# Performance work log

Measured on AMD Instinct MI355X. Metric: run time of the kernel, lower is better.

Reference implementation:

```python
import jax, jax.numpy as jnp
import numpy as np

N = 100000
E = 1600000
F_IN = 128
HID = 64


def setup_inputs() -> dict:
    key = jax.random.key(0)
    ks = jax.random.split(key, 8)
    x = jax.random.normal(ks[0], (N, F_IN), dtype=jnp.float32)
    edge_index = jax.random.randint(ks[1], (2, E), 0, N, dtype=jnp.int32)
    # GCNConv params: weight [in, out] (glorot-ish scale), bias [out]
    W1 = jax.random.normal(ks[2], (F_IN, HID), dtype=jnp.float32) / np.sqrt(F_IN)
    b1 = jnp.zeros((HID,), dtype=jnp.float32)
    W2 = jax.random.normal(ks[3], (HID, HID), dtype=jnp.float32) / np.sqrt(HID)
    b2 = jnp.zeros((HID,), dtype=jnp.float32)
    Wc = jax.random.normal(ks[4], (HID, 1), dtype=jnp.float32) / np.sqrt(HID)
    bc = jnp.zeros((1,), dtype=jnp.float32)
    return {"x": x, "edge_index": edge_index, "W1": W1, "b1": b1,
            "W2": W2, "b2": b2, "Wc": Wc, "bc": bc}


def _gcn_conv(x, src, dst, W, b):
    # PyG GCNConv: h = x @ W, then symmetric-normalized aggregation over
    # edges with self-loops: out[d] = sum_e deg^-1/2[s] deg^-1/2[d] h[s] + b
    n = x.shape[0]
    h = x @ W                                            # [N, out]
    deg = jax.ops.segment_sum(jnp.ones_like(dst, dtype=h.dtype), dst,
                              num_segments=n)            # in-degree incl. self-loops
    dinv = jnp.where(deg > 0, jax.lax.rsqrt(deg), 0.0)   # [N]
    norm = dinv[src] * dinv[dst]                         # [E+N]
    msg = h[src] * norm[:, None]                         # gather + scale
    out = jax.ops.segment_sum(msg, dst, num_segments=n)  # scatter-add
    return out + b


def reference(x, edge_index, W1, b1, W2, b2, Wc, bc):
    n = x.shape[0]
    loop = jnp.arange(n, dtype=edge_index.dtype)
    src = jnp.concatenate([edge_index[0], loop])  # add self-loops
    dst = jnp.concatenate([edge_index[1], loop])
    h = jax.nn.relu(_gcn_conv(x, src, dst, W1, b1))  # dropout in eval mode = identity
    h = jax.nn.relu(_gcn_conv(h, src, dst, W2, b2))
    return (h @ Wc + bc).squeeze(-1)  # [N]
```

## Files before the change

kernel.cpp:

```cpp
#include <hip/hip_runtime.h>


#define FIN 128
#define HIDDEN 64
#define NBUCK 196
#define CAP 9216
#define EPB 8192

typedef __attribute__((ext_vector_type(8))) short bf16x8;
typedef __attribute__((ext_vector_type(4))) float f32x4;

__device__ __forceinline__ unsigned f2bf_pair(float a, float b) {
    unsigned ua = __float_as_uint(a);
    unsigned ub = __float_as_uint(b);
    ua = (ua + 0x7FFFu + ((ua >> 16) & 1u)) >> 16;
    ub = (ub + 0x7FFFu + ((ub >> 16) & 1u)) & 0xFFFF0000u;
    return ua | ub;
}
__device__ __forceinline__ unsigned short f2bf1(float a) {
    unsigned u = __float_as_uint(a);
    return (unsigned short)((u + 0x7FFFu + ((u >> 16) & 1u)) >> 16);
}
#define BF_LO(u) __uint_as_float((u) << 16)
#define BF_HI(u) __uint_as_float((u) & 0xFFFF0000u)

__global__ __launch_bounds__(256) void k_scatter_direct(const int* __restrict__ src,
                                                        const int* __restrict__ dst,
                                                        int* __restrict__ bcursor,
                                                        int* __restrict__ pairs, int e) {
    __shared__ int h[NBUCK], base_s[NBUCK], cur[NBUCK];
    int tid = threadIdx.x;
    if (tid < NBUCK) { h[tid] = 0; cur[tid] = 0; }
    __syncthreads();
    int start = blockIdx.x * EPB;
#pragma unroll
    for (int i = 0; i < EPB / 256; i++) {
        int idx = start + tid + i * 256;
        if (idx < e) atomicAdd(&h[dst[idx] >> 9], 1);
    }
    __syncthreads();
    if (tid < NBUCK && h[tid] > 0) base_s[tid] = atomicAdd(&bcursor[tid], h[tid]);
    __syncthreads();
#pragma unroll
    for (int i = 0; i < EPB / 256; i++) {
        int idx = start + tid + i * 256;
        if (idx < e) {
            int d = dst[idx];
            int b = d >> 9;
            int pos = base_s[b] + atomicAdd(&cur[b], 1);
            if (pos < CAP) pairs[b * CAP + pos] = (src[idx] << 9) | (d & 511);
        }
    }
}

__global__ __launch_bounds__(256) void k_csr_bucket(const int* __restrict__ pairs,
                                                    const int* __restrict__ bcursor,
                                                    int2* __restrict__ rowinfo,
                                                    float* __restrict__ dinv,
                                                    int* __restrict__ csr_src, int n) {
    __shared__ int cnt[512];
    __shared__ int off[512];
    __shared__ int ws2[256];
    int tid = threadIdx.x;
    int b = blockIdx.x;
    int node0 = b << 9;
    cnt[tid] = 0; cnt[tid + 256] = 0;
    __syncthreads();
    int s0 = b * CAP;
    int s1 = s0 + min(bcursor[b], CAP);
    for (int i = s0 + tid; i < s1; i += 256) atomicAdd(&cnt[pairs[i] & 511], 1);
    __syncthreads();
    int c0 = cnt[2 * tid], c1 = cnt[2 * tid + 1];
    int tsum = c0 + c1;
    ws2[tid] = tsum;
    __syncthreads();
    for (int o = 1; o < 256; o <<= 1) {
        int x = 0;
        if (tid >= o) x = ws2[tid - o];
        __syncthreads();
        if (tid >= o) ws2[tid] += x;
        __syncthreads();
    }
    int excl = ws2[tid] - tsum;
    off[2 * tid] = excl;
    off[2 * tid + 1] = excl + c0;
    int n0 = node0 + 2 * tid, n1 = node0 + 2 * tid + 1;
    if (n0 < n) { rowinfo[n0] = make_int2(s0 + excl, c0);      dinv[n0] = rsqrtf((float)c0 + 1.0f); }
    if (n1 < n) { rowinfo[n1] = make_int2(s0 + excl + c0, c1); dinv[n1] = rsqrtf((float)c1 + 1.0f); }
    cnt[2 * tid] = 0; cnt[2 * tid + 1] = 0;
    __syncthreads();
    for (int i = s0 + tid; i < s1; i += 256) {
        int p = pairs[i];
        int l = p & 511;
        int pos = s0 + off[l] + atomicAdd(&cnt[l], 1);
        csr_src[pos] = p >> 9;
    }
}


__global__ __launch_bounds__(256) void k_mfma1(const float4* __restrict__ x4,
                                               const float* __restrict__ w1,
                                               const float* __restrict__ dinv,
                                               uint2* __restrict__ hsb, int n) {
    __shared__ unsigned short sW[64 * 136];
    int tid = threadIdx.x;
#pragma unroll
    for (int i = 0; i < 32; i++) {
        int idx = tid + i * 256;
        int k = idx >> 6, ch = idx & 63;
        sW[ch * 136 + k] = f2bf1(w1[idx]);
    }
    __syncthreads();
    int lane = tid & 63, wave = tid >> 6;
    int quad = lane >> 4, nl = lane & 15;
    int node = blockIdx.x * 64 + wave * 16 + nl;
    int ic = min(node, n - 1);
    const float4* px = x4 + (size_t)ic * 32 + quad * 2;
    bf16x8 bfr[4];
#pragma unroll
    for (int kc = 0; kc < 4; kc++) {
        float4 p = px[kc * 8];
        float4 q = px[kc * 8 + 1];
        union { unsigned u[4]; bf16x8 v; } t;
        t.u[0] = f2bf_pair(p.x, p.y); t.u[1] = f2bf_pair(p.z, p.w);
        t.u[2] = f2bf_pair(q.x, q.y); t.u[3] = f2bf_pair(q.z, q.w);
        bfr[kc] = t.v;
    }
    const bf16x8* sW8 = (const bf16x8*)sW;
    f32x4 a0 = {0.f, 0.f, 0.f, 0.f}, a1 = a0, a2 = a0, a3 = a0;
#pragma unroll
    for (int kc = 0; kc < 4; kc++) {
        int ko = kc * 4 + quad;
        bf16x8 w0 = sW8[(nl +  0) * 17 + ko];
        bf16x8 w1f = sW8[(nl + 16) * 17 + ko];
        bf16x8 w2f = sW8[(nl + 32) * 17 + ko];
        bf16x8 w3f = sW8[(nl + 48) * 17 + ko];
        a0 = __builtin_amdgcn_mfma_f32_16x16x32_bf16(w0,  bfr[kc], a0, 0, 0, 0);
        a1 = __builtin_amdgcn_mfma_f32_16x16x32_bf16(w1f, bfr[kc], a1, 0, 0, 0);
        a2 = __builtin_amdgcn_mfma_f32_16x16x32_bf16(w2f, bfr[kc], a2, 0, 0, 0);
        a3 = __builtin_amdgcn_mfma_f32_16x16x32_bf16(w3f, bfr[kc], a3, 0, 0, 0);
    }
    if (node < n) {
        float s = dinv[node];
        uint2* o = hsb + (size_t)node * 16 + quad;
        o[0]  = make_uint2(f2bf_pair(a0.x * s, a0.y * s), f2bf_pair(a0.z * s, a0.w * s));
        o[4]  = make_uint2(f2bf_pair(a1.x * s, a1.y * s), f2bf_pair(a1.z * s, a1.w * s));
        o[8]  = make_uint2(f2bf_pair(a2.x * s, a2.y * s), f2bf_pair(a2.z * s, a2.w * s));
        o[12] = make_uint2(f2bf_pair(a3.x * s, a3.y * s), f2bf_pair(a3.z * s, a3.w * s));
    }
}

__global__ __launch_bounds__(256) void k_mfma2(const float4* __restrict__ v4,
                                               const float* __restrict__ w2,
                                               const float* __restrict__ dinv,
                                               uint2* __restrict__ hsb, int n) {
    __shared__ unsigned short sW[64 * 72];
    int tid = threadIdx.x;
#pragma unroll
    for (int i = 0; i < 16; i++) {
        int idx = tid + i * 256;
        int k = idx >> 6, ch = idx & 63;
        sW[ch * 72 + k] = f2bf1(w2[idx]);
    }
    __syncthreads();
    int lane = tid & 63, wave = tid >> 6;
    int quad = lane >> 4, nl = lane & 15;
    int node = blockIdx.x * 64 + wave * 16 + nl;
    int ic = min(node, n - 1);
    const float4* px = v4 + (size_t)ic * 16 + quad * 2;
    bf16x8 bfr[2];
#pragma unroll
    for (int kc = 0; kc < 2; kc++) {
        float4 p = px[kc * 8];
        float4 q = px[kc * 8 + 1];
        union { unsigned u[4]; bf16x8 v; } t;
        t.u[0] = f2bf_pair(p.x, p.y); t.u[1] = f2bf_pair(p.z, p.w);
        t.u[2] = f2bf_pair(q.x, q.y); t.u[3] = f2bf_pair(q.z, q.w);
        bfr[kc] = t.v;
    }
    const bf16x8* sW8 = (const bf16x8*)sW;
    f32x4 a0 = {0.f, 0.f, 0.f, 0.f}, a1 = a0, a2 = a0, a3 = a0;
#pragma unroll
    for (int kc = 0; kc < 2; kc++) {
        int ko = kc * 4 + quad;
        bf16x8 w0 = sW8[(nl +  0) * 9 + ko];
        bf16x8 w1f = sW8[(nl + 16) * 9 + ko];
        bf16x8 w2f = sW8[(nl + 32) * 9 + ko];
        bf16x8 w3f = sW8[(nl + 48) * 9 + ko];
        a0 = __builtin_amdgcn_mfma_f32_16x16x32_bf16(w0,  bfr[kc], a0, 0, 0, 0);
        a1 = __builtin_amdgcn_mfma_f32_16x16x32_bf16(w1f, bfr[kc], a1, 0, 0, 0);
        a2 = __builtin_amdgcn_mfma_f32_16x16x32_bf16(w2f, bfr[kc], a2, 0, 0, 0);
        a3 = __builtin_amdgcn_mfma_f32_16x16x32_bf16(w3f, bfr[kc], a3, 0, 0, 0);
    }
    if (node < n) {
        float s = dinv[node];
        uint2* o = hsb + (size_t)node * 16 + quad;
        o[0]  = make_uint2(f2bf_pair(a0.x * s, a0.y * s), f2bf_pair(a0.z * s, a0.w * s));
        o[4]  = make_uint2(f2bf_pair(a1.x * s, a1.y * s), f2bf_pair(a1.z * s, a1.w * s));
        o[8]  = make_uint2(f2bf_pair(a2.x * s, a2.y * s), f2bf_pair(a2.z * s, a2.w * s));
        o[12] = make_uint2(f2bf_pair(a3.x * s, a3.y * s), f2bf_pair(a3.z * s, a3.w * s));
    }
}

__global__ __launch_bounds__(256) void k_agg1_fin(const int2* __restrict__ rowinfo,
                                                  const int* __restrict__ csr_src,
                                                  const uint4* __restrict__ hsb4,
                                                  const float* __restrict__ dinv,
                                                  const float4* __restrict__ b1_4,
                                                  float4* __restrict__ v4out, int n) {
    int lane = threadIdx.x & 63;
    int node = (blockIdx.x * 256 + threadIdx.x) >> 4;
    if (node >= n) return;
    int el = (lane >> 3) & 1, cq = lane & 7;
    int2 rpd = rowinfo[node];
    int start = rpd.x, deg = rpd.y;
    int end = start + deg;
    float4 accA = make_float4(0.f, 0.f, 0.f, 0.f), accB = accA;
    int nr = (deg + 3) >> 2;
    for (int r = 0; r < nr; r++) {
        int base = start + (r << 2);
        int e0 = base + el;
        int e1 = base + 2 + el;
        int s0 = csr_src[min(e0, end - 1)];
        int s1 = csr_src[min(e1, end - 1)];
        float m0 = (e0 < end) ? 1.f : 0.f;
        float m1 = (e1 < end) ? 1.f : 0.f;
        uint4 g0 = hsb4[(size_t)s0 * 8 + cq];
        uint4 g1 = hsb4[(size_t)s1 * 8 + cq];
        accA.x += m0 * BF_LO(g0.x) + m1 * BF_LO(g1.x);
        accA.y += m0 * BF_HI(g0.x) + m1 * BF_HI(g1.x);
        accA.z += m0 * BF_LO(g0.y) + m1 * BF_LO(g1.y);
        accA.w += m0 * BF_HI(g0.y) + m1 * BF_HI(g1.y);
        accB.x += m0 * BF_LO(g0.z) + m1 * BF_LO(g1.z);
        accB.y += m0 * BF_HI(g0.z) + m1 * BF_HI(g1.z);
        accB.z += m0 * BF_LO(g0.w) + m1 * BF_LO(g1.w);
        accB.w += m0 * BF_HI(g0.w) + m1 * BF_HI(g1.w);
    }
    accA.x += __shfl_xor(accA.x, 8); accA.y += __shfl_xor(accA.y, 8);
    accA.z += __shfl_xor(accA.z, 8); accA.w += __shfl_xor(accA.w, 8);
    accB.x += __shfl_xor(accB.x, 8); accB.y += __shfl_xor(accB.y, 8);
    accB.z += __shfl_xor(accB.z, 8); accB.w += __shfl_xor(accB.w, 8);
    if (el == 0) {
        uint4 g = hsb4[(size_t)node * 8 + cq];
        float s = dinv[node];
        float4 bA = b1_4[cq * 2], bB = b1_4[cq * 2 + 1];
        float4 vA, vB;
        vA.x = fmaxf(s * (accA.x + BF_LO(g.x)) + bA.x, 0.f);
        vA.y = fmaxf(s * (accA.y + BF_HI(g.x)) + bA.y, 0.f);
        vA.z = fmaxf(s * (accA.z + BF_LO(g.y)) + bA.z, 0.f);
        vA.w = fmaxf(s * (accA.w + BF_HI(g.y)) + bA.w, 0.f);
        vB.x = fmaxf(s * (accB.x + BF_LO(g.z)) + bB.x, 0.f);
        vB.y = fmaxf(s * (accB.y + BF_HI(g.z)) + bB.y, 0.f);
        vB.z = fmaxf(s * (accB.z + BF_LO(g.w)) + bB.z, 0.f);
        vB.w = fmaxf(s * (accB.w + BF_HI(g.w)) + bB.w, 0.f);
        v4out[(size_t)node * 16 + cq * 2] = vA;
        v4out[(size_t)node * 16 + cq * 2 + 1] = vB;
    }
}

__global__ __launch_bounds__(256) void k_agg2_head(const int2* __restrict__ rowinfo,
                                                   const int* __restrict__ csr_src,
                                                   const uint4* __restrict__ hsb4,
                                                   const float* __restrict__ dinv,
                                                   const float4* __restrict__ b2_4,
                                                   const float4* __restrict__ wc_4,
                                                   const float* __restrict__ bc,
                                                   float* __restrict__ out, int n) {
    int lane = threadIdx.x & 63;
    int node = (blockIdx.x * 256 + threadIdx.x) >> 4;
    if (node >= n) return;
    int el = (lane >> 3) & 1, cq = lane & 7;
    int2 rpd = rowinfo[node];
    int start = rpd.x, deg = rpd.y;
    int end = start + deg;
    float4 accA = make_float4(0.f, 0.f, 0.f, 0.f), accB = accA;
    int nr = (deg + 3) >> 2;
    for (int r = 0; r < nr; r++) {
        int base = start + (r << 2);
        int e0 = base + el;
        int e1 = base + 2 + el;
        int s0 = csr_src[min(e0, end - 1)];
        int s1 = csr_src[min(e1, end - 1)];
        float m0 = (e0 < end) ? 1.f : 0.f;
        float m1 = (e1 < end) ? 1.f : 0.f;
        uint4 g0 = hsb4[(size_t)s0 * 8 + cq];
        uint4 g1 = hsb4[(size_t)s1 * 8 + cq];
        accA.x += m0 * BF_LO(g0.x) + m1 * BF_LO(g1.x);
        accA.y += m0 * BF_HI(g0.x) + m1 * BF_HI(g1.x);
        accA.z += m0 * BF_LO(g0.y) + m1 * BF_LO(g1.y);
        accA.w += m0 * BF_HI(g0.y) + m1 * BF_HI(g1.y);
        accB.x += m0 * BF_LO(g0.z) + m1 * BF_LO(g1.z);
        accB.y += m0 * BF_HI(g0.z) + m1 * BF_HI(g1.z);
        accB.z += m0 * BF_LO(g0.w) + m1 * BF_LO(g1.w);
        accB.w += m0 * BF_HI(g0.w) + m1 * BF_HI(g1.w);
    }
    accA.x += __shfl_xor(accA.x, 8); accA.y += __shfl_xor(accA.y, 8);
    accA.z += __shfl_xor(accA.z, 8); accA.w += __shfl_xor(accA.w, 8);
    accB.x += __shfl_xor(accB.x, 8); accB.y += __shfl_xor(accB.y, 8);
    accB.z += __shfl_xor(accB.z, 8); accB.w += __shfl_xor(accB.w, 8);
    uint4 g = hsb4[(size_t)node * 8 + cq];
    float s = dinv[node];
    float4 bA = b2_4[cq * 2], bB = b2_4[cq * 2 + 1];
    float4 wA = wc_4[cq * 2], wB = wc_4[cq * 2 + 1];
    float t = fmaxf(s * (accA.x + BF_LO(g.x)) + bA.x, 0.f) * wA.x
            + fmaxf(s * (accA.y + BF_HI(g.x)) + bA.y, 0.f) * wA.y
            + fmaxf(s * (accA.z + BF_LO(g.y)) + bA.z, 0.f) * wA.z
            + fmaxf(s * (accA.w + BF_HI(g.y)) + bA.w, 0.f) * wA.w
            + fmaxf(s * (accB.x + BF_LO(g.z)) + bB.x, 0.f) * wB.x
            + fmaxf(s * (accB.y + BF_HI(g.z)) + bB.y, 0.f) * wB.y
            + fmaxf(s * (accB.z + BF_LO(g.w)) + bB.z, 0.f) * wB.z
            + fmaxf(s * (accB.w + BF_HI(g.w)) + bB.w, 0.f) * wB.w;
    t += __shfl_xor(t, 1);
    t += __shfl_xor(t, 2);
    t += __shfl_xor(t, 4);
    if ((lane & 15) == 0) out[node] = t + bc[0];
}

extern "C" void kernel_launch(void* const* d_in, const int* in_sizes, int n_in,
                              void* d_out, int out_size, void* d_ws, size_t ws_size,
                              hipStream_t stream) {
    const float* x  = (const float*)d_in[0];
    const int*   ei = (const int*)d_in[1];
    const float* W1 = (const float*)d_in[2];
    const float* b1 = (const float*)d_in[3];
    const float* W2 = (const float*)d_in[4];
    const float* b2 = (const float*)d_in[5];
    const float* Wc = (const float*)d_in[6];
    const float* bc = (const float*)d_in[7];
    int n = in_sizes[0] / FIN;
    int e = in_sizes[1] / 2;
    const int* srcv = ei;
    const int* dstv = ei + e;

    char* ws = (char*)d_ws;
    float* dinv    = (float*)(ws + 0);
    int2*  rowinfo = (int2*)(ws + (512u << 10));
    int*   csr_src = (int*)(ws + 1536u * 1024);
    int*   bcursor = (int*)(ws + 8800u * 1024);
    uint2* hsb     = (uint2*)(ws + (9u << 20));
    float* v       = (float*)(ws + (22u << 20));
    int*   pairs   = (int*)v;

    int nb_sc   = (e + EPB - 1) / EPB;
    int nb_rows = (n + 63) / 64;
    int nb_agg  = (n + 15) / 16;

    hipMemsetAsync(bcursor, 0, NBUCK * sizeof(int), stream);
    k_scatter_direct<<<nb_sc, 256, 0, stream>>>(srcv, dstv, bcursor, pairs, e);
    k_csr_bucket<<<NBUCK, 256, 0, stream>>>(pairs, bcursor, rowinfo, dinv, csr_src, n);

    k_mfma1<<<nb_rows, 256, 0, stream>>>((const float4*)x, W1, dinv, hsb, n);
    k_agg1_fin<<<nb_agg, 256, 0, stream>>>(rowinfo, csr_src, (const uint4*)hsb,
                                           dinv, (const float4*)b1, (float4*)v, n);
    k_mfma2<<<nb_rows, 256, 0, stream>>>((const float4*)v, W2, dinv, hsb, n);
    k_agg2_head<<<nb_agg, 256, 0, stream>>>(rowinfo, csr_src, (const uint4*)hsb,
                                            dinv, (const float4*)b2, (const float4*)Wc,
                                            bc, (float*)d_out, n);
}
```

Measured before the change: 233.7 us.

## Fuse layer-1 aggregation with layer-2 GEMM through shared memory

Merges the first aggregation kernel and the second MFMA GEMM into one kernel. Each block aggregates 16 nodes into shared memory, then runs the 64x64 bf16 MFMA on them, so the fp32 intermediate activation no longer round-trips through global memory and one launch goes away. Each block now also reconverts W2 to bf16 in shared memory, which is repeated across many more blocks. It also caches dst values in registers in the scatter kernel to avoid a second global load, and adds unroll-2 hints to the gather loops.

```diff
diff --git a/kernel.cpp b/kernel.cpp
--- a/kernel.cpp
+++ b/kernel.cpp
@@ -29,6 +29,7 @@
                                                         int* __restrict__ bcursor,
                                                         int* __restrict__ pairs, int e) {
     __shared__ int h[NBUCK], base_s[NBUCK], cur[NBUCK];
+    int dloc[EPB / 256];
     int tid = threadIdx.x;
     if (tid < NBUCK) { h[tid] = 0; cur[tid] = 0; }
     __syncthreads();
@@ -36,7 +37,9 @@
 #pragma unroll
     for (int i = 0; i < EPB / 256; i++) {
         int idx = start + tid + i * 256;
-        if (idx < e) atomicAdd(&h[dst[idx] >> 9], 1);
+        int d = (idx < e) ? dst[idx] : -1;
+        dloc[i] = d;
+        if (d >= 0) atomicAdd(&h[d >> 9], 1);
     }
     __syncthreads();
     if (tid < NBUCK && h[tid] > 0) base_s[tid] = atomicAdd(&bcursor[tid], h[tid]);
@@ -44,8 +47,8 @@
 #pragma unroll
     for (int i = 0; i < EPB / 256; i++) {
         int idx = start + tid + i * 256;
-        if (idx < e) {
-            int d = dst[idx];
+        int d = dloc[i];
+        if (d >= 0) {
             int b = d >> 9;
             int pos = base_s[b] + atomicAdd(&cur[b], 1);
             if (pos < CAP) pairs[b * CAP + pos] = (src[idx] << 9) | (d & 511);
@@ -150,11 +153,15 @@
     }
 }
 
-__global__ __launch_bounds__(256) void k_mfma2(const float4* __restrict__ v4,
-                                               const float* __restrict__ w2,
-                                               const float* __restrict__ dinv,
-                                               uint2* __restrict__ hsb, int n) {
+__global__ __launch_bounds__(256) void k_agg1_gemm2(const int2* __restrict__ rowinfo,
+                                                    const int* __restrict__ csr_src,
+                                                    const uint4* __restrict__ hsb4,
+                                                    const float* __restrict__ dinv,
+                                                    const float4* __restrict__ b1_4,
+                                                    const float* __restrict__ w2,
+                                                    uint2* __restrict__ hsb2, int n) {
     __shared__ unsigned short sW[64 * 72];
+    __shared__ float sV[16 * 68];
     int tid = threadIdx.x;
 #pragma unroll
     for (int i = 0; i < 16; i++) {
@@ -162,99 +169,80 @@
         int k = idx >> 6, ch = idx & 63;
         sW[ch * 72 + k] = f2bf1(w2[idx]);
     }
-    __syncthreads();
-    int lane = tid & 63, wave = tid >> 6;
+    int lane = tid & 63;
+    int node0 = blockIdx.x * 16;
+    int nloc = tid >> 4;
+    int node = node0 + nloc;
+    int el = (lane >> 3) & 1, cq = lane & 7;
+    if (node < n) {
+        int2 rpd = rowinfo[node];
+        int start = rpd.x, deg = rpd.y;
+        int end = start + deg;
+        float4 accA = make_float4(0.f, 0.f, 0.f, 0.f), accB = accA;
+        int nr = (deg + 3) >> 2;
+#pragma unroll 2
+        for (int r = 0; r < nr; r++) {
+            int base = start + (r << 2);
+            int e0 = base + el;
+            int e1 = base + 2 + el;
+            int s0 = csr_src[min(e0, end - 1)];
+            int s1 = csr_src[min(e1, end - 1)];
+            float m0 = (e0 < end) ? 1.f : 0.f;
+            float m1 = (e1 < end) ? 1.f : 0.f;
+            uint4 g0 = hsb4[(size_t)s0 * 8 + cq];
+            uint4 g1 = hsb4[(size_t)s1 * 8 + cq];
+            accA.x += m0 * BF_LO(g0.x) + m1 * BF_LO(g1.x);
+            accA.y += m0 * BF_HI(g0.x) + m1 * BF_HI(g1.x);
+            accA.z += m0 * BF_LO(g0.y) + m1 * BF_LO(g1.y);
+            accA.w += m0 * BF_HI(g0.y) + m1 * BF_HI(g1.y);
+            accB.x += m0 * BF_LO(g0.z) + m1 * BF_LO(g1.z);
+            accB.y += m0 * BF_HI(g0.z) + m1 * BF_HI(g1.z);
+            accB.z += m0 * BF_LO(g0.w) + m1 * BF_LO(g1.w);
+            accB.w += m0 * BF_HI(g0.w) + m1 * BF_HI(g1.w);
+        }
+        accA.x += __shfl_xor(accA.x, 8); accA.y += __shfl_xor(accA.y, 8);
+        accA.z += __shfl_xor(accA.z, 8); accA.w += __shfl_xor(accA.w, 8);
+        accB.x += __shfl_xor(accB.x, 8); accB.y += __shfl_xor(accB.y, 8);
+        accB.z += __shfl_xor(accB.z, 8); accB.w += __shfl_xor(accB.w, 8);
+        if (el == 0) {
+            uint4 g = hsb4[(size_t)node * 8 + cq];
+            float s = dinv[node];
+            float4 bA = b1_4[cq * 2], bB = b1_4[cq * 2 + 1];
+            float4 vA, vB;
+            vA.x = fmaxf(s * (accA.x + BF_LO(g.x)) + bA.x, 0.f);
+            vA.y = fmaxf(s * (accA.y + BF_HI(g.x)) + bA.y, 0.f);
+            vA.z = fmaxf(s * (accA.z + BF_LO(g.y)) + bA.z, 0.f);
+            vA.w = fmaxf(s * (accA.w + BF_HI(g.y)) + bA.w, 0.f);
+            vB.x = fmaxf(s * (accB.x + BF_LO(g.z)) + bB.x, 0.f);
+            vB.y = fmaxf(s * (accB.y + BF_HI(g.z)) + bB.y, 0.f);
+            vB.z = fmaxf(s * (accB.z + BF_LO(g.w)) + bB.z, 0.f);
+            vB.w = fmaxf(s * (accB.w + BF_HI(g.w)) + bB.w, 0.f);
+            float* vb = sV + nloc * 68 + cq * 8;
+            *(float4*)vb = vA;
+            *(float4*)(vb + 4) = vB;
+        }
+    }
+    __syncthreads();
+    int wave = tid >> 6;
     int quad = lane >> 4, nl = lane & 15;
-    int node = blockIdx.x * 64 + wave * 16 + nl;
-    int ic = min(node, n - 1);
-    const float4* px = v4 + (size_t)ic * 16 + quad * 2;
-    bf16x8 bfr[2];
+    const bf16x8* sW8 = (const bf16x8*)sW;
+    f32x4 acc = {0.f, 0.f, 0.f, 0.f};
 #pragma unroll
     for (int kc = 0; kc < 2; kc++) {
-        float4 p = px[kc * 8];
-        float4 q = px[kc * 8 + 1];
+        const float* vb = sV + nl * 68 + kc * 32 + quad * 8;
+        float4 p = *(const float4*)vb;
+        float4 q = *(const float4*)(vb + 4);
         union { unsigned u[4]; bf16x8 v; } t;
         t.u[0] = f2bf_pair(p.x, p.y); t.u[1] = f2bf_pair(p.z, p.w);
         t.u[2] = f2bf_pair(q.x, q.y); t.u[3] = f2bf_pair(q.z, q.w);
-        bfr[kc] = t.v;
-    }
-    const bf16x8* sW8 = (const bf16x8*)sW;
-    f32x4 a0 = {0.f, 0.f, 0.f, 0.f}, a1 = a0, a2 = a0, a3 = a0;
-#pragma unroll
-    for (int kc = 0; kc < 2; kc++) {
-        int ko = kc * 4 + quad;
-        bf16x8 w0 = sW8[(nl +  0) * 9 + ko];
-        bf16x8 w1f = sW8[(nl + 16) * 9 + ko];
-        bf16x8 w2f = sW8[(nl + 32) * 9 + ko];
-        bf16x8 w3f = sW8[(nl + 48) * 9 + ko];
-        a0 = __builtin_amdgcn_mfma_f32_16x16x32_bf16(w0,  bfr[kc], a0, 0, 0, 0);
-        a1 = __builtin_amdgcn_mfma_f32_16x16x32_bf16(w1f, bfr[kc], a1, 0, 0, 0);
-        a2 = __builtin_amdgcn_mfma_f32_16x16x32_bf16(w2f, bfr[kc], a2, 0, 0, 0);
-        a3 = __builtin_amdgcn_mfma_f32_16x16x32_bf16(w3f, bfr[kc], a3, 0, 0, 0);
-    }
-    if (node < n) {
-        float s = dinv[node];
-        uint2* o = hsb + (size_t)node * 16 + quad;
-        o[0]  = make_uint2(f2bf_pair(a0.x * s, a0.y * s), f2bf_pair(a0.z * s, a0.w * s));
-        o[4]  = make_uint2(f2bf_pair(a1.x * s, a1.y * s), f2bf_pair(a1.z * s, a1.w * s));
-        o[8]  = make_uint2(f2bf_pair(a2.x * s, a2.y * s), f2bf_pair(a2.z * s, a2.w * s));
-        o[12] = make_uint2(f2bf_pair(a3.x * s, a3.y * s), f2bf_pair(a3.z * s, a3.w * s));
-    }
-}
-
-__global__ __launch_bounds__(256) void k_agg1_fin(const int2* __restrict__ rowinfo,
-                                                  const int* __restrict__ csr_src,
-                                                  const uint4* __restrict__ hsb4,
-                                                  const float* __restrict__ dinv,
-                                                  const float4* __restrict__ b1_4,
-                                                  float4* __restrict__ v4out, int n) {
-    int lane = threadIdx.x & 63;
-    int node = (blockIdx.x * 256 + threadIdx.x) >> 4;
-    if (node >= n) return;
-    int el = (lane >> 3) & 1, cq = lane & 7;
-    int2 rpd = rowinfo[node];
-    int start = rpd.x, deg = rpd.y;
-    int end = start + deg;
-    float4 accA = make_float4(0.f, 0.f, 0.f, 0.f), accB = accA;
-    int nr = (deg + 3) >> 2;
-    for (int r = 0; r < nr; r++) {
-        int base = start + (r << 2);
-        int e0 = base + el;
-        int e1 = base + 2 + el;
-        int s0 = csr_src[min(e0, end - 1)];
-        int s1 = csr_src[min(e1, end - 1)];
-        float m0 = (e0 < end) ? 1.f : 0.f;
-        float m1 = (e1 < end) ? 1.f : 0.f;
-        uint4 g0 = hsb4[(size_t)s0 * 8 + cq];
-        uint4 g1 = hsb4[(size_t)s1 * 8 + cq];
-        accA.x += m0 * BF_LO(g0.x) + m1 * BF_LO(g1.x);
-        accA.y += m0 * BF_HI(g0.x) + m1 * BF_HI(g1.x);
-        accA.z += m0 * BF_LO(g0.y) + m1 * BF_LO(g1.y);
-        accA.w += m0 * BF_HI(g0.y) + m1 * BF_HI(g1.y);
-        accB.x += m0 * BF_LO(g0.z) + m1 * BF_LO(g1.z);
-        accB.y += m0 * BF_HI(g0.z) + m1 * BF_HI(g1.z);
-        accB.z += m0 * BF_LO(g0.w) + m1 * BF_LO(g1.w);
-        accB.w += m0 * BF_HI(g0.w) + m1 * BF_HI(g1.w);
-    }
-    accA.x += __shfl_xor(accA.x, 8); accA.y += __shfl_xor(accA.y, 8);
-    accA.z += __shfl_xor(accA.z, 8); accA.w += __shfl_xor(accA.w, 8);
-    accB.x += __shfl_xor(accB.x, 8); accB.y += __shfl_xor(accB.y, 8);
-    accB.z += __shfl_xor(accB.z, 8); accB.w += __shfl_xor(accB.w, 8);
-    if (el == 0) {
-        uint4 g = hsb4[(size_t)node * 8 + cq];
-        float s = dinv[node];
-        float4 bA = b1_4[cq * 2], bB = b1_4[cq * 2 + 1];
-        float4 vA, vB;
-        vA.x = fmaxf(s * (accA.x + BF_LO(g.x)) + bA.x, 0.f);
-        vA.y = fmaxf(s * (accA.y + BF_HI(g.x)) + bA.y, 0.f);
-        vA.z = fmaxf(s * (accA.z + BF_LO(g.y)) + bA.z, 0.f);
-        vA.w = fmaxf(s * (accA.w + BF_HI(g.y)) + bA.w, 0.f);
-        vB.x = fmaxf(s * (accB.x + BF_LO(g.z)) + bB.x, 0.f);
-        vB.y = fmaxf(s * (accB.y + BF_HI(g.z)) + bB.y, 0.f);
-        vB.z = fmaxf(s * (accB.z + BF_LO(g.w)) + bB.z, 0.f);
-        vB.w = fmaxf(s * (accB.w + BF_HI(g.w)) + bB.w, 0.f);
-        v4out[(size_t)node * 16 + cq * 2] = vA;
-        v4out[(size_t)node * 16 + cq * 2 + 1] = vB;
+        bf16x8 a = sW8[(wave * 16 + nl) * 9 + kc * 4 + quad];
+        acc = __builtin_amdgcn_mfma_f32_16x16x32_bf16(a, t.v, acc, 0, 0, 0);
+    }
+    int onode = node0 + nl;
+    if (onode < n) {
+        float s = dinv[onode];
+        hsb2[(size_t)onode * 16 + wave * 4 + quad] =
+            make_uint2(f2bf_pair(acc.x * s, acc.y * s), f2bf_pair(acc.z * s, acc.w * s));
     }
 }
 
@@ -275,6 +263,7 @@
     int end = start + deg;
     float4 accA = make_float4(0.f, 0.f, 0.f, 0.f), accB = accA;
     int nr = (deg + 3) >> 2;
+#pragma unroll 2
     for (int r = 0; r < nr; r++) {
         int base = start + (r << 2);
         int e0 = base + el;
@@ -337,9 +326,9 @@
     int2*  rowinfo = (int2*)(ws + (512u << 10));
     int*   csr_src = (int*)(ws + 1536u * 1024);
     int*   bcursor = (int*)(ws + 8800u * 1024);
-    uint2* hsb     = (uint2*)(ws + (9u << 20));
-    float* v       = (float*)(ws + (22u << 20));
-    int*   pairs   = (int*)v;
+    uint2* hsb1    = (uint2*)(ws + (9u << 20));
+    uint2* hsb2    = (uint2*)(ws + (22u << 20));
+    int*   pairs   = (int*)hsb2;
 
     int nb_sc   = (e + EPB - 1) / EPB;
     int nb_rows = (n + 63) / 64;
@@ -349,11 +338,10 @@
     k_scatter_direct<<<nb_sc, 256, 0, stream>>>(srcv, dstv, bcursor, pairs, e);
     k_csr_bucket<<<NBUCK, 256, 0, stream>>>(pairs, bcursor, rowinfo, dinv, csr_src, n);
 
-    k_mfma1<<<nb_rows, 256, 0, stream>>>((const float4*)x, W1, dinv, hsb, n);
-    k_agg1_fin<<<nb_agg, 256, 0, stream>>>(rowinfo, csr_src, (const uint4*)hsb,
-                                           dinv, (const float4*)b1, (float4*)v, n);
-    k_mfma2<<<nb_rows, 256, 0, stream>>>((const float4*)v, W2, dinv, hsb, n);
-    k_agg2_head<<<nb_agg, 256, 0, stream>>>(rowinfo, csr_src, (const uint4*)hsb,
+    k_mfma1<<<nb_rows, 256, 0, stream>>>((const float4*)x, W1, dinv, hsb1, n);
+    k_agg1_gemm2<<<nb_agg, 256, 0, stream>>>(rowinfo, csr_src, (const uint4*)hsb1,
+                                             dinv, (const float4*)b1, W2, hsb2, n);
+    k_agg2_head<<<nb_agg, 256, 0, stream>>>(rowinfo, csr_src, (const uint4*)hsb2,
                                             dinv, (const float4*)b2, (const float4*)Wc,
                                             bc, (float*)d_out, n);
 }
```

Measured after the change: 217.5 us. 6.9% less time.
